# Optimization experiments

Hardware: AMD Instinct MI355X
Metric: run time of the kernel (lower is better)

Reference implementation:

```python
import jax, jax.numpy as jnp
import numpy as np

H = 1024      # hidden_size
V = 50257     # output_size (vocab)
L = 100       # max_length


def setup_inputs() -> dict:
    key = jax.random.key(0)
    ks = jax.random.split(key, 14)
    s = 0.02
    return {
        "token": jax.random.randint(ks[0], (1,), 0, V),
        "hidden": jax.random.normal(ks[1], (1, 1, H), jnp.float32),
        "encoder_outputs": jax.random.normal(ks[2], (L, H), jnp.float32),
        "embedding": jax.random.normal(ks[3], (V, H), jnp.float32) * s,
        "attn_w": jax.random.normal(ks[4], (L, 2 * H), jnp.float32) * s,
        "attn_b": jnp.zeros((L,), jnp.float32),
        "comb_w": jax.random.normal(ks[5], (H, 2 * H), jnp.float32) * s,
        "comb_b": jnp.zeros((H,), jnp.float32),
        "w_ih": jax.random.normal(ks[6], (3 * H, H), jnp.float32) * s,
        "w_hh": jax.random.normal(ks[7], (3 * H, H), jnp.float32) * s,
        "b_ih": jnp.zeros((3 * H,), jnp.float32),
        "b_hh": jnp.zeros((3 * H,), jnp.float32),
        "out_w": jax.random.normal(ks[8], (V, H), jnp.float32) * s,
        "out_b": jnp.zeros((V,), jnp.float32),
    }


def reference(token, hidden, encoder_outputs, embedding, attn_w, attn_b,
              comb_w, comb_b, w_ih, w_hh, b_ih, b_hh, out_w, out_b):
    # embedding lookup; dropout is identity in eval mode
    emb = embedding[token]                                   # [1, H]
    h0 = hidden[0]                                           # [1, H]
    # attention over encoder positions
    attn_in = jnp.concatenate([emb, h0], axis=1)             # [1, 2H]
    attn_weights = jax.nn.softmax(attn_in @ attn_w.T + attn_b, axis=1)  # [1, L]
    attn_applied = attn_weights @ encoder_outputs            # [1, H]
    # combine + relu
    x = jnp.concatenate([emb, attn_applied], axis=1) @ comb_w.T + comb_b  # [1, H]
    x = jax.nn.relu(x)
    # single GRU cell step (PyTorch gate order: r, z, n)
    gi = x @ w_ih.T + b_ih                                   # [1, 3H]
    gh = h0 @ w_hh.T + b_hh                                  # [1, 3H]
    ir, iz, in_ = jnp.split(gi, 3, axis=1)
    hr, hz, hn = jnp.split(gh, 3, axis=1)
    r = jax.nn.sigmoid(ir + hr)
    z = jax.nn.sigmoid(iz + hz)
    n = jnp.tanh(in_ + r * hn)
    h_new = (1.0 - z) * n + z * h0                           # [1, H]
    # output projection + log_softmax
    output = jax.nn.log_softmax(h_new @ out_w.T + out_b, axis=1)  # [1, V]
    return output, h_new[None], attn_weights
```

## Files before the change

### kernel.cpp

```cpp
#include <hip/hip_runtime.h>
#include <hip/hip_bf16.h>

#define H 1024
#define V 50257
#define L 100
#define NDB 2048


__device__ __forceinline__ float wave_sum(float v) {
    #pragma unroll
    for (int off = 32; off > 0; off >>= 1) v += __shfl_down(v, off, 64);
    return v;
}

__device__ __forceinline__ float dot1024(const float4* w, const float4* x, int lane) {
    float acc = 0.f;
    #pragma unroll
    for (int j = 0; j < 4; j++) {
        float4 a = w[lane + 64 * j];
        float4 b = x[lane + 64 * j];
        acc += a.x * b.x + a.y * b.y + a.z * b.z + a.w * b.w;
    }
    return acc;
}


__global__ void kA_logits(const int* token, const float* hidden, const float* embedding,
                          const float* attn_w, const float* attn_b, float* ws_log) {
    int lane = threadIdx.x;
    int r = blockIdx.x;
    const float4* e4 = (const float4*)(embedding + (size_t)token[0] * H);
    const float4* h4 = (const float4*)hidden;
    const float4* wr = (const float4*)(attn_w + (size_t)r * (2 * H));
    float acc = dot1024(wr, e4, lane) + dot1024(wr + 256, h4, lane);
    acc = wave_sum(acc);
    if (lane == 0) ws_log[r] = acc + attn_b[r];
}


__global__ void kS_softmax_apply(const float* ws_log, const float* enc,
                                 float* ws_app, float* out_attnw) {
    __shared__ float red[8];
    __shared__ float aw_s[128];
    __shared__ float part[4][64];
    int t = threadIdx.x, lane = t & 63, wv = t >> 6;

    float x = (t < L) ? ws_log[t] : -1e30f;
    float mv = x;
    #pragma unroll
    for (int off = 32; off > 0; off >>= 1) mv = fmaxf(mv, __shfl_down(mv, off, 64));
    if (lane == 0) red[wv] = mv;
    __syncthreads();
    float m = fmaxf(fmaxf(red[0], red[1]), fmaxf(red[2], red[3]));
    float e = (t < L) ? expf(x - m) : 0.f;
    float sv = wave_sum(e);
    if (lane == 0) red[4 + wv] = sv;
    __syncthreads();
    float s = red[4] + red[5] + red[6] + red[7];
    float aw = e / s;
    if (t < 128) aw_s[t] = aw;
    if (blockIdx.x == 0 && t < L) out_attnw[t] = aw;
    __syncthreads();

    int h = blockIdx.x * 64 + lane;
    float acc = 0.f;
    #pragma unroll
    for (int i = 0; i < 25; i++) {
        int l = wv * 25 + i;
        acc += aw_s[l] * enc[l * H + h];
    }
    part[wv][lane] = acc;
    __syncthreads();
    if (wv == 0)
        ws_app[h] = part[0][lane] + part[1][lane] + part[2][lane] + part[3][lane];
}


__global__ void kComb(const int* token, const float* embedding, const float* ws_app,
                      const float* comb_w, const float* comb_b, float* ws_x) {
    int lane = threadIdx.x & 63, wv = threadIdx.x >> 6;
    int r = blockIdx.x * 4 + wv;
    const float4* e4 = (const float4*)(embedding + (size_t)token[0] * H);
    const float4* a4 = (const float4*)ws_app;
    const float4* wr = (const float4*)(comb_w + (size_t)r * (2 * H));
    float acc = dot1024(wr, e4, lane) + dot1024(wr + 256, a4, lane);
    acc = wave_sum(acc);
    if (lane == 0) ws_x[r] = fmaxf(acc + comb_b[r], 0.0f);
}


__global__ void kGRU(const float* ws_x, const float* hidden,
                     const float* w_ih, const float* w_hh,
                     const float* b_ih, const float* b_hh,
                     float* out_h, float* ws_hn) {
    __shared__ float sh[2][2][3];
    int lane = threadIdx.x & 63, wv = threadIdx.x >> 6;
    int pair = wv >> 1, isGh = wv & 1;
    int h = blockIdx.x * 2 + pair;
    const float4* vec = isGh ? (const float4*)hidden : (const float4*)ws_x;
    const float*  Wm  = isGh ? w_hh : w_ih;
    float a0 = dot1024((const float4*)(Wm + (size_t)h * H), vec, lane);
    float a1 = dot1024((const float4*)(Wm + (size_t)(H + h) * H), vec, lane);
    float a2 = dot1024((const float4*)(Wm + (size_t)(2 * H + h) * H), vec, lane);
    a0 = wave_sum(a0); a1 = wave_sum(a1); a2 = wave_sum(a2);
    if (lane == 0) { sh[pair][isGh][0] = a0; sh[pair][isGh][1] = a1; sh[pair][isGh][2] = a2; }
    __syncthreads();
    if (!isGh && lane == 0) {
        float ir = sh[pair][0][0] + b_ih[h], iz = sh[pair][0][1] + b_ih[H + h],
              in_ = sh[pair][0][2] + b_ih[2 * H + h];
        float hr = sh[pair][1][0] + b_hh[h], hz = sh[pair][1][1] + b_hh[H + h],
              hn = sh[pair][1][2] + b_hh[2 * H + h];
        float r = 1.f / (1.f + expf(-(ir + hr)));
        float z = 1.f / (1.f + expf(-(iz + hz)));
        float n = tanhf(in_ + r * hn);
        float h0 = hidden[h];
        float v = (1.f - z) * n + z * h0;
        out_h[h] = v;
        ws_hn[h] = v;
    }
}


__global__ void kD_outproj(const float* hn, const float* out_w, const float* out_b,
                           float* out_logits, float* ws_pm, float* ws_ps) {
    __shared__ float sm[4], ss[4];
    int lane = threadIdx.x & 63;
    int wv   = threadIdx.x >> 6;
    const float4* h4 = (const float4*)hn;
    float4 h0 = h4[lane], h1 = h4[lane + 64], h2 = h4[lane + 128], h3 = h4[lane + 192];
    float m = -1e30f, s = 0.f;
    int wid = blockIdx.x * 4 + wv;
    for (int r0 = wid * 2; r0 < V; r0 += NDB * 8) {
        float acc[2] = {0.f, 0.f};
        #pragma unroll
        for (int i = 0; i < 2; i++) {
            int r = r0 + i;
            if (r < V) {
                const float4* wr = (const float4*)(out_w + (size_t)r * H);
                float4 a = wr[lane], b = wr[lane + 64], c = wr[lane + 128], d = wr[lane + 192];
                acc[i] = a.x * h0.x + a.y * h0.y + a.z * h0.z + a.w * h0.w
                       + b.x * h1.x + b.y * h1.y + b.z * h1.z + b.w * h1.w
                       + c.x * h2.x + c.y * h2.y + c.z * h2.z + c.w * h2.w
                       + d.x * h3.x + d.y * h3.y + d.z * h3.z + d.w * h3.w;
            }
        }
        #pragma unroll
        for (int off = 32; off > 0; off >>= 1) {
            acc[0] += __shfl_down(acc[0], off, 64);
            acc[1] += __shfl_down(acc[1], off, 64);
        }
        if (lane == 0) {
            #pragma unroll
            for (int i = 0; i < 2; i++) {
                int r = r0 + i;
                if (r < V) {
                    float lg = acc[i] + out_b[r];
                    out_logits[r] = lg;
                    float nm = fmaxf(m, lg);
                    s = s * expf(m - nm) + expf(lg - nm);
                    m = nm;
                }
            }
        }
    }
    if (lane == 0) { sm[wv] = m; ss[wv] = s; }
    __syncthreads();
    if (threadIdx.x == 0) {
        m = sm[0]; s = ss[0];
        #pragma unroll
        for (int i = 1; i < 4; i++) {
            float nm = fmaxf(m, sm[i]);
            s = s * expf(m - nm) + ss[i] * expf(sm[i] - nm);
            m = nm;
        }
        ws_pm[blockIdx.x] = m;
        ws_ps[blockIdx.x] = s;
    }
}


__global__ void kE_finalize(const float* ws_pm, const float* ws_ps, float* out) {
    __shared__ float sm[4], ss[4], fm, fs;
    int t = threadIdx.x;
    float m = -1e30f, s = 0.f;
    for (int i = t; i < NDB; i += 256) {
        float pm = ws_pm[i], ps = ws_ps[i];
        float nm = fmaxf(m, pm);
        s = s * expf(m - nm) + ps * expf(pm - nm);
        m = nm;
    }
    #pragma unroll
    for (int off = 32; off > 0; off >>= 1) {
        float om = __shfl_down(m, off, 64);
        float os = __shfl_down(s, off, 64);
        float nm = fmaxf(m, om);
        s = s * expf(m - nm) + os * expf(om - nm);
        m = nm;
    }
    int lane = t & 63, wv = t >> 6;
    if (lane == 0) { sm[wv] = m; ss[wv] = s; }
    __syncthreads();
    if (t == 0) {
        m = sm[0]; s = ss[0];
        #pragma unroll
        for (int i = 1; i < 4; i++) {
            float nm = fmaxf(m, sm[i]);
            s = s * expf(m - nm) + ss[i] * expf(sm[i] - nm);
            m = nm;
        }
        fm = m; fs = logf(s);
    }
    __syncthreads();
    float M = fm, LS = fs;
    for (int v = blockIdx.x * 256 + t; v < V; v += gridDim.x * 256)
        out[v] = out[v] - M - LS;
}


extern "C" void kernel_launch(void* const* d_in, const int* in_sizes, int n_in,
                              void* d_out, int out_size, void* d_ws, size_t ws_size,
                              hipStream_t stream) {
    const int*   token     = (const int*)d_in[0];
    const float* hidden    = (const float*)d_in[1];
    const float* enc       = (const float*)d_in[2];
    const float* embedding = (const float*)d_in[3];
    const float* attn_w    = (const float*)d_in[4];
    const float* attn_b    = (const float*)d_in[5];
    const float* comb_w    = (const float*)d_in[6];
    const float* comb_b    = (const float*)d_in[7];
    const float* w_ih      = (const float*)d_in[8];
    const float* w_hh      = (const float*)d_in[9];
    const float* b_ih      = (const float*)d_in[10];
    const float* b_hh      = (const float*)d_in[11];
    const float* out_w     = (const float*)d_in[12];
    const float* out_b     = (const float*)d_in[13];

    float* out = (float*)d_out;
    float* ws  = (float*)d_ws;
    float* ws_log = ws;
    float* ws_app = ws + 128;
    float* ws_x   = ws + 1152;
    float* ws_pm  = ws + 2176;
    float* ws_ps  = ws + 4224;
    float* ws_hn  = ws + 6272;

    kA_logits<<<dim3(L), dim3(64), 0, stream>>>(token, hidden, embedding,
                                                attn_w, attn_b, ws_log);
    kS_softmax_apply<<<dim3(16), dim3(256), 0, stream>>>(ws_log, enc, ws_app, out + V + H);
    kComb<<<dim3(256), dim3(256), 0, stream>>>(token, embedding, ws_app,
                                               comb_w, comb_b, ws_x);
    kGRU<<<dim3(512), dim3(256), 0, stream>>>(ws_x, hidden, w_ih, w_hh, b_ih, b_hh,
                                              out + V, ws_hn);
    kD_outproj<<<dim3(NDB), dim3(256), 0, stream>>>(ws_hn, out_w, out_b, out, ws_pm, ws_ps);
    kE_finalize<<<dim3(128), dim3(256), 0, stream>>>(ws_pm, ws_ps, out);
}
```

Baseline: 58.43 us.

## Fuse attention, combine and hidden-side GRU matvec into fewer kernel launches

Merges the attention-logits kernel with the w_hh @ h0 matvec, since neither depends on earlier stages. Softmax, attention-apply and the combine matvec now run in one kernel. Each of its 128 blocks recomputes the softmax and the full 100x1024 weighted sum redundantly into shared memory, which removes a launch and the ws_app round trip. The launch count drops from six to five and the serial dependency chain gets shorter, in exchange for redundant reads of encoder_outputs across blocks.

Measured after the change: 63.75 us. +9.1%, slower.

```diff
diff --git a/kernel.cpp b/kernel.cpp
--- a/kernel.cpp
+++ b/kernel.cpp
@@ -25,24 +25,34 @@
 }
 
 
-__global__ void kA_logits(const int* token, const float* hidden, const float* embedding,
-                          const float* attn_w, const float* attn_b, float* ws_log) {
-    int lane = threadIdx.x;
-    int r = blockIdx.x;
+__global__ void k1_head(const int* token, const float* hidden, const float* embedding,
+                        const float* attn_w, const float* attn_b,
+                        const float* w_hh, const float* b_hh,
+                        float* ws_log, float* ws_gh) {
+    int lane = threadIdx.x & 63, wv = threadIdx.x >> 6;
     const float4* e4 = (const float4*)(embedding + (size_t)token[0] * H);
     const float4* h4 = (const float4*)hidden;
-    const float4* wr = (const float4*)(attn_w + (size_t)r * (2 * H));
-    float acc = dot1024(wr, e4, lane) + dot1024(wr + 256, h4, lane);
-    acc = wave_sum(acc);
-    if (lane == 0) ws_log[r] = acc + attn_b[r];
-}
-
-
-__global__ void kS_softmax_apply(const float* ws_log, const float* enc,
-                                 float* ws_app, float* out_attnw) {
+    if (blockIdx.x < 25) {
+        int r = blockIdx.x * 4 + wv;
+        const float4* wr = (const float4*)(attn_w + (size_t)r * (2 * H));
+        float acc = dot1024(wr, e4, lane) + dot1024(wr + 256, h4, lane);
+        acc = wave_sum(acc);
+        if (lane == 0) ws_log[r] = acc + attn_b[r];
+    } else {
+        int r = (blockIdx.x - 25) * 4 + wv;
+        const float4* wr = (const float4*)(w_hh + (size_t)r * H);
+        float acc = wave_sum(dot1024(wr, h4, lane));
+        if (lane == 0) ws_gh[r] = acc + b_hh[r];
+    }
+}
+
+
+__global__ void k2_mid(const int* token, const float* ws_log, const float* enc,
+                       const float* embedding, const float* comb_w, const float* comb_b,
+                       float* ws_x, float* out_attnw) {
     __shared__ float red[8];
-    __shared__ float aw_s[128];
-    __shared__ float part[4][64];
+    __shared__ float aw[128];
+    __shared__ float4 app4[256];
     int t = threadIdx.x, lane = t & 63, wv = t >> 6;
 
     float x = (t < L) ? ws_log[t] : -1e30f;
@@ -57,59 +67,50 @@
     if (lane == 0) red[4 + wv] = sv;
     __syncthreads();
     float s = red[4] + red[5] + red[6] + red[7];
-    float aw = e / s;
-    if (t < 128) aw_s[t] = aw;
-    if (blockIdx.x == 0 && t < L) out_attnw[t] = aw;
-    __syncthreads();
-
-    int h = blockIdx.x * 64 + lane;
-    float acc = 0.f;
-    #pragma unroll
-    for (int i = 0; i < 25; i++) {
-        int l = wv * 25 + i;
-        acc += aw_s[l] * enc[l * H + h];
-    }
-    part[wv][lane] = acc;
-    __syncthreads();
-    if (wv == 0)
-        ws_app[h] = part[0][lane] + part[1][lane] + part[2][lane] + part[3][lane];
-}
-
-
-__global__ void kComb(const int* token, const float* embedding, const float* ws_app,
-                      const float* comb_w, const float* comb_b, float* ws_x) {
+    float a = e / s;
+    if (t < 128) aw[t] = a;
+    if (blockIdx.x == 0 && t < L) out_attnw[t] = a;
+    __syncthreads();
+
+    {
+        const float4* enc4 = (const float4*)enc;
+        float4 acc4 = make_float4(0.f, 0.f, 0.f, 0.f);
+        #pragma unroll 4
+        for (int l = 0; l < L; l++) {
+            float w = aw[l];
+            float4 ev = enc4[l * 256 + t];
+            acc4.x += w * ev.x; acc4.y += w * ev.y;
+            acc4.z += w * ev.z; acc4.w += w * ev.w;
+        }
+        app4[t] = acc4;
+    }
+    __syncthreads();
+
+    const float4* e4 = (const float4*)(embedding + (size_t)token[0] * H);
+    #pragma unroll
+    for (int k = 0; k < 2; k++) {
+        int r = blockIdx.x * 8 + wv * 2 + k;
+        const float4* wr = (const float4*)(comb_w + (size_t)r * (2 * H));
+        float acc = dot1024(wr, e4, lane) + dot1024(wr + 256, app4, lane);
+        acc = wave_sum(acc);
+        if (lane == 0) ws_x[r] = fmaxf(acc + comb_b[r], 0.0f);
+    }
+}
+
+
+__global__ void k3_gru(const float* ws_x, const float* hidden, const float* ws_gh,
+                       const float* w_ih, const float* b_ih, const float* b_hh,
+                       float* out_h, float* ws_hn) {
     int lane = threadIdx.x & 63, wv = threadIdx.x >> 6;
-    int r = blockIdx.x * 4 + wv;
-    const float4* e4 = (const float4*)(embedding + (size_t)token[0] * H);
-    const float4* a4 = (const float4*)ws_app;
-    const float4* wr = (const float4*)(comb_w + (size_t)r * (2 * H));
-    float acc = dot1024(wr, e4, lane) + dot1024(wr + 256, a4, lane);
-    acc = wave_sum(acc);
-    if (lane == 0) ws_x[r] = fmaxf(acc + comb_b[r], 0.0f);
-}
-
-
-__global__ void kGRU(const float* ws_x, const float* hidden,
-                     const float* w_ih, const float* w_hh,
-                     const float* b_ih, const float* b_hh,
-                     float* out_h, float* ws_hn) {
-    __shared__ float sh[2][2][3];
-    int lane = threadIdx.x & 63, wv = threadIdx.x >> 6;
-    int pair = wv >> 1, isGh = wv & 1;
-    int h = blockIdx.x * 2 + pair;
-    const float4* vec = isGh ? (const float4*)hidden : (const float4*)ws_x;
-    const float*  Wm  = isGh ? w_hh : w_ih;
-    float a0 = dot1024((const float4*)(Wm + (size_t)h * H), vec, lane);
-    float a1 = dot1024((const float4*)(Wm + (size_t)(H + h) * H), vec, lane);
-    float a2 = dot1024((const float4*)(Wm + (size_t)(2 * H + h) * H), vec, lane);
+    int h = blockIdx.x * 4 + wv;
+    const float4* x4 = (const float4*)ws_x;
+    float a0 = dot1024((const float4*)(w_ih + (size_t)h * H), x4, lane);
+    float a1 = dot1024((const float4*)(w_ih + (size_t)(H + h) * H), x4, lane);
+    float a2 = dot1024((const float4*)(w_ih + (size_t)(2 * H + h) * H), x4, lane);
     a0 = wave_sum(a0); a1 = wave_sum(a1); a2 = wave_sum(a2);
-    if (lane == 0) { sh[pair][isGh][0] = a0; sh[pair][isGh][1] = a1; sh[pair][isGh][2] = a2; }
-    __syncthreads();
-    if (!isGh && lane == 0) {
-        float ir = sh[pair][0][0] + b_ih[h], iz = sh[pair][0][1] + b_ih[H + h],
-              in_ = sh[pair][0][2] + b_ih[2 * H + h];
-        float hr = sh[pair][1][0] + b_hh[h], hz = sh[pair][1][1] + b_hh[H + h],
-              hn = sh[pair][1][2] + b_hh[2 * H + h];
+    if (lane == 0) {
+        float ir = a0 + b_ih[h], iz = a1 + b_ih[H + h], in_ = a2 + b_ih[2 * H + h];
+        float hr = ws_gh[h] , hz = ws_gh[H + h],  hn = ws_gh[2 * H + h];
         float r = 1.f / (1.f + expf(-(ir + hr)));
         float z = 1.f / (1.f + expf(-(iz + hz)));
         float n = tanhf(in_ + r * hn);
@@ -238,19 +239,19 @@
     float* out = (float*)d_out;
     float* ws  = (float*)d_ws;
     float* ws_log = ws;
-    float* ws_app = ws + 128;
-    float* ws_x   = ws + 1152;
-    float* ws_pm  = ws + 2176;
-    float* ws_ps  = ws + 4224;
-    float* ws_hn  = ws + 6272;
-
-    kA_logits<<<dim3(L), dim3(64), 0, stream>>>(token, hidden, embedding,
-                                                attn_w, attn_b, ws_log);
-    kS_softmax_apply<<<dim3(16), dim3(256), 0, stream>>>(ws_log, enc, ws_app, out + V + H);
-    kComb<<<dim3(256), dim3(256), 0, stream>>>(token, embedding, ws_app,
-                                               comb_w, comb_b, ws_x);
-    kGRU<<<dim3(512), dim3(256), 0, stream>>>(ws_x, hidden, w_ih, w_hh, b_ih, b_hh,
-                                              out + V, ws_hn);
+    float* ws_gh  = ws + 128;
+    float* ws_x   = ws + 3200;
+    float* ws_pm  = ws + 4224;
+    float* ws_ps  = ws + 6272;
+    float* ws_hn  = ws + 8320;
+
+    k1_head<<<dim3(793), dim3(256), 0, stream>>>(token, hidden, embedding,
+                                                 attn_w, attn_b, w_hh, b_hh,
+                                                 ws_log, ws_gh);
+    k2_mid<<<dim3(128), dim3(256), 0, stream>>>(token, ws_log, enc, embedding,
+                                                comb_w, comb_b, ws_x, out + V + H);
+    k3_gru<<<dim3(256), dim3(256), 0, stream>>>(ws_x, hidden, ws_gh, w_ih, b_ih, b_hh,
+                                                out + V, ws_hn);
     kD_outproj<<<dim3(NDB), dim3(256), 0, stream>>>(ws_hn, out_w, out_b, out, ws_pm, ws_ps);
     kE_finalize<<<dim3(128), dim3(256), 0, stream>>>(ws_pm, ws_ps, out);
 }
```
